# Kernel optimization log

Hardware: AMD Instinct MI355X
Metric: run time of the kernel (lower is better)

Reference implementation:

```python
import math
import jax, jax.numpy as jnp
import numpy as np

C, H, R, PD = 256, 6, 32, 16
HEAD_SCALE = 1.0 / math.sqrt(R)


def setup_inputs() -> dict:
    key = jax.random.key(0)
    ks = jax.random.split(key, 8)
    B, Lp1 = 8, 4097
    feats = jax.random.normal(ks[0], (B, Lp1, C), dtype=jnp.float32)
    # params (stored [in, out] for x @ W)
    Wq = jax.random.normal(ks[1], (C, H * R), dtype=jnp.float32) / math.sqrt(C)
    Wk = jax.random.normal(ks[2], (C, H * R), dtype=jnp.float32) / math.sqrt(C)
    Wpi = jax.random.normal(ks[3], (C, PD), dtype=jnp.float32) / math.sqrt(C)
    bpi = jnp.zeros((PD,), jnp.float32)
    Wpj = jax.random.normal(ks[4], (C, PD), dtype=jnp.float32) / math.sqrt(C)
    bpj = jnp.zeros((PD,), jnp.float32)
    Wd = jax.random.normal(ks[5], (C, 1), dtype=jnp.float32) / math.sqrt(C)
    bd = jnp.zeros((1,), jnp.float32)
    alpha_pair = jnp.float32(0.5)
    logit_scale = jnp.float32(1.0)
    return {"feats": feats, "Wq": Wq, "Wk": Wk, "Wpi": Wpi, "bpi": bpi,
            "Wpj": Wpj, "bpj": bpj, "Wd": Wd, "bd": bd,
            "alpha_pair": alpha_pair, "logit_scale": logit_scale}


def _fold_vertices(feats):
    x = feats[:, 1:]                      # drop first token
    B, L, Cc = x.shape
    return x.reshape(B, L // 2, 2, Cc).mean(axis=2)  # [B, N, C]


def reference(feats, Wq, Wk, Wpi, bpi, Wpj, bpj, Wd, bd, alpha_pair, logit_scale):
    x = _fold_vertices(feats)             # [B, N, C]
    B, N, _ = x.shape
    Q = (x @ Wq).reshape(B, N, H, R)
    K = (x @ Wk).reshape(B, N, H, R)
    # sum over heads fused into one contraction (math-equal to per-head scores summed)
    S = jnp.einsum('bnhr,bmhr->bnm', Q, K) * HEAD_SCALE   # [B, N, N]
    a_i = jax.nn.relu(x @ Wpi + bpi)      # [B, N, PD]
    b_j = jax.nn.relu(x @ Wpj + bpj)
    S = S + jnp.maximum(alpha_pair, 0.0) * jnp.einsum('bnd,bmd->bnm', a_i, b_j)
    d = (x @ Wd + bd)[..., 0]             # [B, N]
    idx = jnp.arange(N)
    S = S.at[:, idx, idx].add(d)
    return S * jnp.maximum(logit_scale, 0.01)
```

## Files before the change

### kernel.cpp

```cpp
#include <hip/hip_runtime.h>
#include <hip/hip_bf16.h>
#include <stdint.h>

typedef __attribute__((ext_vector_type(8))) short short8;
typedef __attribute__((ext_vector_type(4))) short short4v;
typedef __attribute__((ext_vector_type(4))) float f32x4;
typedef __attribute__((ext_vector_type(4))) unsigned uint4v;

#define NB 8
#define NN 2048
#define CC 256
#define LP1 4097
#define HR 192
#define PDim 16
#define KP 224
#define NPAD 448
#define HEAD_SCALE 0.17677669529663689f

#define GLOAD16(g, l) __builtin_amdgcn_global_load_lds( \
    (const __attribute__((address_space(1))) unsigned int*)(g), \
    (__attribute__((address_space(3))) unsigned int*)(l), 16, 0, 0)

static __device__ __forceinline__ unsigned short bf16bits(float f) {
    __hip_bfloat16 h = __float2bfloat16(f);
    return *(unsigned short*)&h;
}

__global__ __launch_bounds__(256) void k0_prep(
    const float* __restrict__ Wq, const float* __restrict__ Wk,
    const float* __restrict__ Wpi, const float* __restrict__ Wpj,
    const float* __restrict__ Wd,
    __hip_bfloat16* __restrict__ WT,
    unsigned* __restrict__ Ppad, unsigned* __restrict__ Rpad)
{
    const int WTN = NPAD*CC;
    const int PV  = NB*NN*2;
    int i = blockIdx.x*blockDim.x + threadIdx.x;
    if (i < WTN) {
        int c = i >> 8, k = i & 255;
        float v;
        if (c < HR)                 v = Wq[k*HR + c] * HEAD_SCALE;
        else if (c < 2*HR)          v = Wk[k*HR + (c-HR)];
        else if (c < 2*HR+PDim)     v = Wpi[k*PDim + (c-2*HR)];
        else if (c < 2*HR+2*PDim)   v = Wpj[k*PDim + (c-2*HR-PDim)];
        else if (c == 416)          v = Wd[k];
        else                        v = 0.f;
        WT[i] = __float2bfloat16(v);
    } else {
        int j = i - WTN;
        unsigned* arr = (j < PV) ? Ppad : Rpad;
        int q = (j < PV) ? j : j - PV;
        int row = q >> 1, of = 104 + (q & 1)*4;
        *(uint4v*)(arr + (size_t)row*(KP/2) + of) = (uint4v){0,0,0,0};
    }
}

__global__ __launch_bounds__(256, 3) void ka_proj(
    const float* __restrict__ feats, const __hip_bfloat16* __restrict__ WT,
    const float* __restrict__ bpi, const float* __restrict__ bpj,
    const float* __restrict__ bd, const float* __restrict__ alpha_pair,
    __hip_bfloat16* __restrict__ P, __hip_bfloat16* __restrict__ R,
    float* __restrict__ dvec)
{
    __shared__ __hip_bfloat16 lds[32*256];

    int t = threadIdx.x;
    int lane = t & 63;
    int w = t >> 6;
    int l15 = lane & 15, lg = lane >> 4;
    int row0 = blockIdx.x * 32;
    int b = row0 >> 11;
    int n0loc = row0 & (NN-1);

    {
        int r = t >> 3, cg = t & 7;
        size_t fb = ((size_t)b*LP1 + 1 + 2*(size_t)(n0loc + r))*CC + cg*32;
#pragma unroll
        for (int s = 0; s < 4; ++s) {
            float4 a0 = *(const float4*)(feats + fb + s*8);
            float4 a1 = *(const float4*)(feats + fb + s*8 + 4);
            float4 c0 = *(const float4*)(feats + fb + CC + s*8);
            float4 c1 = *(const float4*)(feats + fb + CC + s*8 + 4);
            unsigned short h[8];
            h[0] = bf16bits(0.5f*(a0.x + c0.x));
            h[1] = bf16bits(0.5f*(a0.y + c0.y));
            h[2] = bf16bits(0.5f*(a0.z + c0.z));
            h[3] = bf16bits(0.5f*(a0.w + c0.w));
            h[4] = bf16bits(0.5f*(a1.x + c1.x));
            h[5] = bf16bits(0.5f*(a1.y + c1.y));
            h[6] = bf16bits(0.5f*(a1.z + c1.z));
            h[7] = bf16bits(0.5f*(a1.w + c1.w));
            int slot = (cg*4 + s) ^ (r & 7);
            *(short8*)((char*)lds + r*512 + slot*16) = *(const short8*)h;
        }
    }
    __syncthreads();

    const __hip_bfloat16* pB[7];
#pragma unroll
    for (int ni = 0; ni < 7; ++ni)
        pB[ni] = WT + (size_t)(w*112 + ni*16 + l15)*CC + lg*8;

    f32x4 acc[7][2];
#pragma unroll
    for (int ni = 0; ni < 7; ++ni)
#pragma unroll
        for (int mi = 0; mi < 2; ++mi)
            acc[ni][mi] = (f32x4){0.f, 0.f, 0.f, 0.f};

    int arow[2];
#pragma unroll
    for (int mi = 0; mi < 2; ++mi) arow[mi] = (mi*16 + l15)*512;
    int rx = l15 & 7;

#pragma unroll
    for (int kk = 0; kk < 8; ++kk) {
        short8 a[2], bb[7];
        int slotb = ((kk*4 + lg) ^ rx) << 4;
#pragma unroll
        for (int mi = 0; mi < 2; ++mi)
            a[mi] = *(const short8*)((const char*)lds + arow[mi] + slotb);
#pragma unroll
        for (int ni = 0; ni < 7; ++ni) bb[ni] = *(const short8*)(pB[ni] + kk*32);
#pragma unroll
        for (int ni = 0; ni < 7; ++ni)
#pragma unroll
            for (int mi = 0; mi < 2; ++mi)
                acc[ni][mi] = __builtin_amdgcn_mfma_f32_16x16x32_bf16(
                    bb[ni], a[mi], acc[ni][mi], 0, 0, 0);
    }

    float alpha_eff = fmaxf(alpha_pair[0], 0.f);
    float bd0 = bd[0];
#pragma unroll
    for (int ni = 0; ni < 7; ++ni) {
        int cb = w*112 + ni*16 + lg*4;
#pragma unroll
        for (int mi = 0; mi < 2; ++mi) {
            int n = n0loc + mi*16 + l15;
            size_t rb = ((size_t)b*NN + n)*KP;
            f32x4 v = acc[ni][mi];
            if (cb < HR) {
                short4v h;
#pragma unroll
                for (int j = 0; j < 4; ++j) h[j] = (short)bf16bits(v[j]);
                *(short4v*)(P + rb + cb) = h;
            } else if (cb < 2*HR) {
                short4v h;
#pragma unroll
                for (int j = 0; j < 4; ++j) h[j] = (short)bf16bits(v[j]);
                *(short4v*)(R + rb + (cb - HR)) = h;
            } else if (cb < 2*HR + PDim) {
                int pc = cb - 2*HR;
                short4v h;
#pragma unroll
                for (int j = 0; j < 4; ++j)
                    h[j] = (short)bf16bits(fmaxf(v[j] + bpi[pc+j], 0.f) * alpha_eff);
                *(short4v*)(P + rb + HR + pc) = h;
            } else if (cb < 2*HR + 2*PDim) {
                int pc = cb - 2*HR - PDim;
                short4v h;
#pragma unroll
                for (int j = 0; j < 4; ++j)
                    h[j] = (short)bf16bits(fmaxf(v[j] + bpj[pc+j], 0.f));
                *(short4v*)(R + rb + HR + pc) = h;
            } else if (cb == 416) {
                dvec[(size_t)b*NN + n] = v[0] + bd0;
            }
        }
    }
}

__global__ __launch_bounds__(256, 4) void kb_pair(
    const __hip_bfloat16* __restrict__ P, const __hip_bfloat16* __restrict__ R,
    const float* __restrict__ dvec, const float* __restrict__ logit_scale,
    float* __restrict__ out)
{
    __shared__ __hip_bfloat16 ldsA[2][128*32];
    __shared__ __hip_bfloat16 ldsB[2][128*32];

    int t = threadIdx.x;
    int lane = t & 63;
    int w = t >> 6;
    int wr = w >> 1, wc = w & 1;
    int l15 = lane & 15, lg = lane >> 4;

    int hw = blockIdx.x;
    int b = hw & 7;
    int within = hw >> 3;
    int m0 = (within & 15) << 7;
    int n0 = (within >> 4) << 7;

    const char* srcA[2];
    const char* srcB[2];
#pragma unroll
    for (int i = 0; i < 2; ++i) {
        int row   = i*64 + (t >> 2);
        int scolb = ((t & 3) << 4) ^ ((row & 3) << 4);
        srcA[i] = (const char*)(P + ((size_t)b*NN + n0 + row)*KP) + scolb;
        srcB[i] = (const char*)(R + ((size_t)b*NN + m0 + row)*KP) + scolb;
    }
    int ldst = w * 1024;

    int abyte = (wr*64 + l15)*64 + ((lg ^ (l15 & 3)) << 4);
    int bbyte = (wc*64 + l15)*64 + ((lg ^ (l15 & 3)) << 4);

    f32x4 acc[4][4];
#pragma unroll
    for (int ni = 0; ni < 4; ++ni)
#pragma unroll
        for (int mi = 0; mi < 4; ++mi)
            acc[ni][mi] = (f32x4){0.f, 0.f, 0.f, 0.f};

#pragma unroll
    for (int i = 0; i < 2; ++i) {
        GLOAD16(srcA[i], (char*)(&ldsA[0][0]) + i*4096 + ldst);
        GLOAD16(srcB[i], (char*)(&ldsB[0][0]) + i*4096 + ldst);
    }
#pragma unroll
    for (int i = 0; i < 2; ++i) {
        GLOAD16(srcA[i] + 64, (char*)(&ldsA[1][0]) + i*4096 + ldst);
        GLOAD16(srcB[i] + 64, (char*)(&ldsB[1][0]) + i*4096 + ldst);
    }

#pragma unroll
    for (int s = 0; s < 7; ++s) {
        if (s < 6) asm volatile("s_waitcnt vmcnt(4)" ::: "memory");
        else       asm volatile("s_waitcnt vmcnt(0)" ::: "memory");
        __builtin_amdgcn_s_barrier();
        __builtin_amdgcn_sched_barrier(0);

        const int buf = s & 1;
        short8 a[4], bb[4];
#pragma unroll
        for (int mi = 0; mi < 4; ++mi)
            a[mi] = *(const short8*)((const char*)(&ldsA[buf][0]) + abyte + mi*1024);
#pragma unroll
        for (int ni = 0; ni < 4; ++ni)
            bb[ni] = *(const short8*)((const char*)(&ldsB[buf][0]) + bbyte + ni*1024);
#pragma unroll
        for (int ni = 0; ni < 4; ++ni)
#pragma unroll
            for (int mi = 0; mi < 4; ++mi)
                acc[ni][mi] = __builtin_amdgcn_mfma_f32_16x16x32_bf16(
                    bb[ni], a[mi], acc[ni][mi], 0, 0, 0);

        __builtin_amdgcn_sched_barrier(0);
        __builtin_amdgcn_s_barrier();
        if (s + 2 < 7) {
            size_t kof = (size_t)(s + 2) * 64;
#pragma unroll
            for (int i = 0; i < 2; ++i) {
                GLOAD16(srcA[i] + kof, (char*)(&ldsA[buf][0]) + i*4096 + ldst);
                GLOAD16(srcB[i] + kof, (char*)(&ldsB[buf][0]) + i*4096 + ldst);
            }
        }
    }

    float ls = fmaxf(logit_scale[0], 0.01f);
    bool diag_tile = (n0 == m0);
#pragma unroll
    for (int ni = 0; ni < 4; ++ni) {
#pragma unroll
        for (int mi = 0; mi < 4; ++mi) {
            int orow  = n0 + wr*64 + mi*16 + l15;
            int cbase = m0 + wc*64 + ni*16 + lg*4;
            f32x4 v = acc[ni][mi];
            if (diag_tile) {
                int dj = orow - cbase;
                if (dj >= 0 && dj < 4) v[dj] += dvec[(size_t)b*NN + orow];
            }
            f32x4 o;
#pragma unroll
            for (int j = 0; j < 4; ++j) o[j] = v[j] * ls;
            *(f32x4*)(out + ((size_t)b*NN + orow)*NN + cbase) = o;
        }
    }
}

extern "C" void kernel_launch(void* const* d_in, const int* in_sizes, int n_in,
                              void* d_out, int out_size, void* d_ws, size_t ws_size,
                              hipStream_t stream)
{
    const float* feats = (const float*)d_in[0];
    const float* Wq    = (const float*)d_in[1];
    const float* Wk    = (const float*)d_in[2];
    const float* Wpi   = (const float*)d_in[3];
    const float* bpi   = (const float*)d_in[4];
    const float* Wpj   = (const float*)d_in[5];
    const float* bpj   = (const float*)d_in[6];
    const float* Wd    = (const float*)d_in[7];
    const float* bd    = (const float*)d_in[8];
    const float* alpha = (const float*)d_in[9];
    const float* lsc   = (const float*)d_in[10];

    char* ws = (char*)d_ws;
    __hip_bfloat16* WT = (__hip_bfloat16*)(ws);
    __hip_bfloat16* P  = (__hip_bfloat16*)(ws + 229376);
    __hip_bfloat16* R  = (__hip_bfloat16*)(ws + 7569408);
    float*          dv = (float*)(ws + 14909440);

    k0_prep<<<704, 256, 0, stream>>>(Wq, Wk, Wpi, Wpj, Wd,
                                     WT, (unsigned*)P, (unsigned*)R);
    ka_proj<<<512, 256, 0, stream>>>(feats, WT, bpi, bpj, bd, alpha, P, R, dv);
    kb_pair<<<2048, 256, 0, stream>>>(P, R, dv, lsc, (float*)d_out);
}
```

Before: 69.23 us.

## Stage projection weights through double-buffered LDS with async global-to-LDS loads

The projection kernel used to read weight fragments directly from global memory inside the K loop. It now streams 448x32 weight tiles into two LDS buffers with global_load_lds, prefetching two K-steps ahead and guarding each step with vmcnt waits and barriers. The goal is to hide global-load latency and keep the B loads coalesced. In exchange the kernel uses about 64KB of LDS per block, adds two barriers per iteration, and lowers the occupancy hint from 3 to 2 blocks.

Result: faster. 66.98 us (-3.2%).

```diff
diff --git a/kernel.cpp b/kernel.cpp
--- a/kernel.cpp
+++ b/kernel.cpp
@@ -55,14 +55,15 @@
     }
 }
 
-__global__ __launch_bounds__(256, 3) void ka_proj(
+__global__ __launch_bounds__(256, 2) void ka_proj(
     const float* __restrict__ feats, const __hip_bfloat16* __restrict__ WT,
     const float* __restrict__ bpi, const float* __restrict__ bpj,
     const float* __restrict__ bd, const float* __restrict__ alpha_pair,
     __hip_bfloat16* __restrict__ P, __hip_bfloat16* __restrict__ R,
     float* __restrict__ dvec)
 {
-    __shared__ __hip_bfloat16 lds[32*256];
+    __shared__ __hip_bfloat16 ldsA[32*256];
+    __shared__ __hip_bfloat16 ldsB[2][448*32];
 
     int t = threadIdx.x;
     int lane = t & 63;
@@ -71,6 +72,21 @@
     int row0 = blockIdx.x * 32;
     int b = row0 >> 11;
     int n0loc = row0 & (NN-1);
+
+    const char* srcB[7];
+#pragma unroll
+    for (int i = 0; i < 7; ++i) {
+        int row   = i*64 + (t >> 2);
+        int scolb = ((t & 3) << 4) ^ ((row & 3) << 4);
+        srcB[i] = (const char*)WT + (size_t)row*512 + scolb;
+    }
+    char* B0 = (char*)&ldsB[0][0];
+    int ldstB = w * 1024;
+
+#pragma unroll
+    for (int i = 0; i < 7; ++i) GLOAD16(srcB[i],      B0 + i*4096 + ldstB);
+#pragma unroll
+    for (int i = 0; i < 7; ++i) GLOAD16(srcB[i] + 64, B0 + 28672 + i*4096 + ldstB);
 
     {
         int r = t >> 3, cg = t & 7;
@@ -91,15 +107,10 @@
             h[6] = bf16bits(0.5f*(a1.z + c1.z));
             h[7] = bf16bits(0.5f*(a1.w + c1.w));
             int slot = (cg*4 + s) ^ (r & 7);
-            *(short8*)((char*)lds + r*512 + slot*16) = *(const short8*)h;
+            *(short8*)((char*)ldsA + r*512 + slot*16) = *(const short8*)h;
         }
     }
     __syncthreads();
-
-    const __hip_bfloat16* pB[7];
-#pragma unroll
-    for (int ni = 0; ni < 7; ++ni)
-        pB[ni] = WT + (size_t)(w*112 + ni*16 + l15)*CC + lg*8;
 
     f32x4 acc[7][2];
 #pragma unroll
@@ -112,22 +123,39 @@
 #pragma unroll
     for (int mi = 0; mi < 2; ++mi) arow[mi] = (mi*16 + l15)*512;
     int rx = l15 & 7;
+    int bbase = (w*112 + l15)*64 + ((lg ^ (l15 & 3)) << 4);
 
 #pragma unroll
     for (int kk = 0; kk < 8; ++kk) {
+        if (kk < 7) asm volatile("s_waitcnt vmcnt(7)" ::: "memory");
+        else        asm volatile("s_waitcnt vmcnt(0)" ::: "memory");
+        __builtin_amdgcn_s_barrier();
+        __builtin_amdgcn_sched_barrier(0);
+
+        const int buf = kk & 1;
         short8 a[2], bb[7];
         int slotb = ((kk*4 + lg) ^ rx) << 4;
 #pragma unroll
         for (int mi = 0; mi < 2; ++mi)
-            a[mi] = *(const short8*)((const char*)lds + arow[mi] + slotb);
-#pragma unroll
-        for (int ni = 0; ni < 7; ++ni) bb[ni] = *(const short8*)(pB[ni] + kk*32);
+            a[mi] = *(const short8*)((const char*)ldsA + arow[mi] + slotb);
+#pragma unroll
+        for (int ni = 0; ni < 7; ++ni)
+            bb[ni] = *(const short8*)(B0 + buf*28672 + bbase + ni*1024);
 #pragma unroll
         for (int ni = 0; ni < 7; ++ni)
 #pragma unroll
             for (int mi = 0; mi < 2; ++mi)
                 acc[ni][mi] = __builtin_amdgcn_mfma_f32_16x16x32_bf16(
                     bb[ni], a[mi], acc[ni][mi], 0, 0, 0);
+
+        __builtin_amdgcn_sched_barrier(0);
+        __builtin_amdgcn_s_barrier();
+        if (kk + 2 < 8) {
+            size_t kof = (size_t)(kk + 2) * 64;
+#pragma unroll
+            for (int i = 0; i < 7; ++i)
+                GLOAD16(srcB[i] + kof, B0 + buf*28672 + i*4096 + ldstB);
+        }
     }
 
     float alpha_eff = fmaxf(alpha_pair[0], 0.f);
```

## Stage projection weights through LDS and change the score-kernel LDS swizzle

Applied to the files above, without the earlier changes.

The projection kernel no longer reads its weight fragments straight from global memory into registers for each MFMA. It now loads each 448x32 K-slice of the transposed weights cooperatively into LDS with a swizzled layout, prefetching the next slice into registers while the current one is consumed, with barriers around the LDS rewrite. The score kernel's LDS swizzle changes from row&3 to (row>>2)&3 to reduce bank conflicts on fragment reads. The cost is two extra barriers per K step and more LDS use, which may lower occupancy of the projection kernel.

Result: faster. 64.26 us (-7.2%).

```diff
diff --git a/kernel.cpp b/kernel.cpp
--- a/kernel.cpp
+++ b/kernel.cpp
@@ -62,7 +62,8 @@
     __hip_bfloat16* __restrict__ P, __hip_bfloat16* __restrict__ R,
     float* __restrict__ dvec)
 {
-    __shared__ __hip_bfloat16 lds[32*256];
+    __shared__ __hip_bfloat16 ldsA[32*256];
+    __shared__ __hip_bfloat16 ldsB[448*32];
 
     int t = threadIdx.x;
     int lane = t & 63;
@@ -71,6 +72,20 @@
     int row0 = blockIdx.x * 32;
     int b = row0 >> 11;
     int n0loc = row0 & (NN-1);
+
+    int scol = (((t & 3) ^ ((t >> 4) & 3)) << 4);
+    const char* srcB[7];
+    int wofB[7];
+#pragma unroll
+    for (int i = 0; i < 7; ++i) {
+        int row = i*64 + (t >> 2);
+        srcB[i] = (const char*)WT + (size_t)row*512 + scol;
+        wofB[i] = row*64 + ((t & 3) << 4);
+    }
+
+    uint4v st[7];
+#pragma unroll
+    for (int i = 0; i < 7; ++i) st[i] = *(const uint4v*)(srcB[i]);
 
     {
         int r = t >> 3, cg = t & 7;
@@ -91,15 +106,14 @@
             h[6] = bf16bits(0.5f*(a1.z + c1.z));
             h[7] = bf16bits(0.5f*(a1.w + c1.w));
             int slot = (cg*4 + s) ^ (r & 7);
-            *(short8*)((char*)lds + r*512 + slot*16) = *(const short8*)h;
-        }
-    }
+            *(short8*)((char*)ldsA + r*512 + slot*16) = *(const short8*)h;
+        }
+    }
+
+#pragma unroll
+    for (int i = 0; i < 7; ++i)
+        *(uint4v*)((char*)ldsB + wofB[i]) = st[i];
     __syncthreads();
-
-    const __hip_bfloat16* pB[7];
-#pragma unroll
-    for (int ni = 0; ni < 7; ++ni)
-        pB[ni] = WT + (size_t)(w*112 + ni*16 + l15)*CC + lg*8;
 
     f32x4 acc[7][2];
 #pragma unroll
@@ -112,22 +126,37 @@
 #pragma unroll
     for (int mi = 0; mi < 2; ++mi) arow[mi] = (mi*16 + l15)*512;
     int rx = l15 & 7;
+    int bbase = (w*112 + l15)*64 + ((lg ^ ((l15 >> 2) & 3)) << 4);
 
 #pragma unroll
     for (int kk = 0; kk < 8; ++kk) {
+        if (kk < 7) {
+#pragma unroll
+            for (int i = 0; i < 7; ++i)
+                st[i] = *(const uint4v*)(srcB[i] + (size_t)(kk + 1)*64);
+        }
         short8 a[2], bb[7];
         int slotb = ((kk*4 + lg) ^ rx) << 4;
 #pragma unroll
         for (int mi = 0; mi < 2; ++mi)
-            a[mi] = *(const short8*)((const char*)lds + arow[mi] + slotb);
-#pragma unroll
-        for (int ni = 0; ni < 7; ++ni) bb[ni] = *(const short8*)(pB[ni] + kk*32);
+            a[mi] = *(const short8*)((const char*)ldsA + arow[mi] + slotb);
+#pragma unroll
+        for (int ni = 0; ni < 7; ++ni)
+            bb[ni] = *(const short8*)((const char*)ldsB + bbase + ni*1024);
 #pragma unroll
         for (int ni = 0; ni < 7; ++ni)
 #pragma unroll
             for (int mi = 0; mi < 2; ++mi)
                 acc[ni][mi] = __builtin_amdgcn_mfma_f32_16x16x32_bf16(
                     bb[ni], a[mi], acc[ni][mi], 0, 0, 0);
+
+        __syncthreads();
+        if (kk < 7) {
+#pragma unroll
+            for (int i = 0; i < 7; ++i)
+                *(uint4v*)((char*)ldsB + wofB[i]) = st[i];
+            __syncthreads();
+        }
     }
 
     float alpha_eff = fmaxf(alpha_pair[0], 0.f);
@@ -193,17 +222,19 @@
 
     const char* srcA[2];
     const char* srcB[2];
-#pragma unroll
-    for (int i = 0; i < 2; ++i) {
-        int row   = i*64 + (t >> 2);
-        int scolb = ((t & 3) << 4) ^ ((row & 3) << 4);
-        srcA[i] = (const char*)(P + ((size_t)b*NN + n0 + row)*KP) + scolb;
-        srcB[i] = (const char*)(R + ((size_t)b*NN + m0 + row)*KP) + scolb;
+    {
+        int scolb = (((t & 3) ^ ((t >> 4) & 3)) << 4);
+#pragma unroll
+        for (int i = 0; i < 2; ++i) {
+            int row = i*64 + (t >> 2);
+            srcA[i] = (const char*)(P + ((size_t)b*NN + n0 + row)*KP) + scolb;
+            srcB[i] = (const char*)(R + ((size_t)b*NN + m0 + row)*KP) + scolb;
+        }
     }
     int ldst = w * 1024;
 
-    int abyte = (wr*64 + l15)*64 + ((lg ^ (l15 & 3)) << 4);
-    int bbyte = (wc*64 + l15)*64 + ((lg ^ (l15 & 3)) << 4);
+    int abyte = (wr*64 + l15)*64 + ((lg ^ ((l15 >> 2) & 3)) << 4);
+    int bbyte = (wc*64 + l15)*64 + ((lg ^ ((l15 >> 2) & 3)) << 4);
 
     f32x4 acc[4][4];
 #pragma unroll
```
